# Performance work log

Hardware: AMD Instinct MI355X
Metric: run time of the kernel (lower is better)

Reference implementation:

```python
import jax, jax.numpy as jnp
import numpy as np

SEQ_LEN = 12
E, H, BOTTLE = 64, 128, 1024
G, P = 64, 24
B = G * P
EPS = 1e-12  # F.normalize eps


def setup_inputs() -> dict:
    key = jax.random.key(0)
    ks = jax.random.split(key, 24)
    r = lambda k, s: (jax.random.normal(k, s, dtype=jnp.float32) * 0.1)
    starts = np.arange(G, dtype=np.int64) * P
    seq_start_end = jnp.asarray(np.stack([starts, starts + P], axis=1))
    return {
        'last_pos': jax.random.normal(ks[0], (B, 2), dtype=jnp.float32),
        'last_pos_rel': jax.random.normal(ks[1], (B, 2), dtype=jnp.float32),
        'h0': jax.random.normal(ks[2], (1, B, H), dtype=jnp.float32),
        'c0': jax.random.normal(ks[3], (1, B, H), dtype=jnp.float32),
        'seq_start_end': seq_start_end,
        # decoder spatial embedding Linear(2, E)
        'W_emb': r(ks[4], (E, 2)), 'b_emb': r(ks[5], (E,)),
        # LSTM(E -> H), gates ordered i,f,g,o as in torch
        'W_ih': r(ks[6], (4 * H, E)), 'W_hh': r(ks[7], (4 * H, H)),
        'b_ih': r(ks[8], (4 * H,)), 'b_hh': r(ks[9], (4 * H,)),
        # hidden2pos Linear(H, 2)
        'W_pos': r(ks[10], (2, H)), 'b_pos': r(ks[11], (2,)),
        # pool_net spatial embedding Linear(2, E)
        'Wp_emb': r(ks[12], (E, 2)), 'bp_emb': r(ks[13], (E,)),
        # pool_net mlp_pre_pool: (E+H)->512->1024, ReLU
        'Wp1': r(ks[14], (512, E + H)), 'bp1': r(ks[15], (512,)),
        'Wp2': r(ks[16], (BOTTLE, 512)), 'bp2': r(ks[17], (BOTTLE,)),
        # decoder mlp: (H+BOTTLE)->1024->H, ReLU
        'Wm1': r(ks[18], (1024, H + BOTTLE)), 'bm1': r(ks[19], (1024,)),
        'Wm2': r(ks[20], (H, 1024)), 'bm2': r(ks[21], (H,)),
    }


def reference(last_pos, last_pos_rel, h0, c0, seq_start_end,
              W_emb, b_emb, W_ih, W_hh, b_ih, b_hh, W_pos, b_pos,
              Wp_emb, bp_emb, Wp1, bp1, Wp2, bp2, Wm1, bm1, Wm2, bm2):
    batch = last_pos.shape[0]
    n_grp = seq_start_end.shape[0]
    n_ped = batch // n_grp  # equal contiguous groups -> static reshape
    h_dim = h0.shape[-1]

    def pool_net(h, pos):
        # h: [B,H], pos: [B,2]; groups are contiguous slices of size n_ped
        pos_g = pos.reshape(n_grp, n_ped, 2)
        hid_g = h.reshape(n_grp, n_ped, h_dim)
        # rel[g,i,j] = pos[g,j] - pos[g,i]  (torch repeat semantics)
        rel = pos_g[:, None, :, :] - pos_g[:, :, None, :]  # [G,P,P,2]
        nrm = jnp.linalg.norm(rel, axis=-1, keepdims=True)
        rel = rel / jnp.maximum(nrm, EPS)
        emb = rel @ Wp_emb.T + bp_emb                       # [G,P,P,E]
        hid_b = jnp.broadcast_to(hid_g[:, None, :, :], (n_grp, n_ped, n_ped, h_dim))
        x = jnp.concatenate([emb, hid_b], axis=-1)          # [G,P,P,E+H]
        x = jax.nn.relu(x @ Wp1.T + bp1)
        x = jax.nn.relu(x @ Wp2.T + bp2)                    # [G,P,P,1024]
        return jnp.max(x, axis=2).reshape(batch, -1)        # max over j

    def lstm_step(x, h, c):
        gates = x @ W_ih.T + b_ih + h @ W_hh.T + b_hh
        i, f, g, o = jnp.split(gates, 4, axis=-1)
        c = jax.nn.sigmoid(f) * c + jax.nn.sigmoid(i) * jnp.tanh(g)
        h = jax.nn.sigmoid(o) * jnp.tanh(c)
        return h, c

    def step(carry, _):
        h, c, lp, dec_in = carry
        h, c = lstm_step(dec_in, h, c)
        rel_pos = h @ W_pos.T + b_pos          # [B,2]
        curr_pos = rel_pos + lp
        pool_h = pool_net(h, curr_pos)         # [B,1024]
        dh = jnp.concatenate([h, pool_h], axis=1)
        dh = jax.nn.relu(dh @ Wm1.T + bm1)
        h = jax.nn.relu(dh @ Wm2.T + bm2)      # refreshed hidden state
        dec_in = rel_pos @ W_emb.T + b_emb
        return (h, c, curr_pos, dec_in), rel_pos

    dec_in0 = last_pos_rel @ W_emb.T + b_emb
    (h, c, lp, di), rels = jax.lax.scan(
        step, (h0[0], c0[0], last_pos, dec_in0), None, length=SEQ_LEN)
    return rels, h[None]  # ([seq_len,B,2], [1,B,H])
```

## Files before the change

kernel.cpp:

```cpp
#include <hip/hip_runtime.h>
#include <hip/hip_bf16.h>

typedef __attribute__((ext_vector_type(4))) float f32x4;
typedef __attribute__((ext_vector_type(8))) _Float16 f16x8;

static __device__ __forceinline__ unsigned short h2u(_Float16 h) {
  union { _Float16 h; unsigned short u; } v; v.h = h; return v.u;
}

#define MFMA16(a, b, c) __builtin_amdgcn_mfma_f32_16x16x32_f16(a, b, c, 0, 0, 0)


__global__ void build_wg(const float* __restrict__ W_ih, const float* __restrict__ W_hh,
                         _Float16* __restrict__ Wg) {
  int i = blockIdx.x * 256 + threadIdx.x;
  if (i < 512 * 192) {
    int rp = i / 192, k = i % 192;
    int u = rp >> 2, gate = rp & 3;
    int sr = gate * 128 + u;
    float v = (k < 64) ? W_ih[sr * 64 + k] : W_hh[sr * 128 + (k - 64)];
    _Float16 h = (_Float16)v;
    Wg[i] = h;
    Wg[512 * 192 + i] = (_Float16)(v - (float)h);
  }
}

__global__ void build_wp1b(const float* __restrict__ Wp1, _Float16* __restrict__ W) {
  int i = blockIdx.x * 256 + threadIdx.x;
  if (i < 512 * 128) {
    int r = i >> 7, k = i & 127;
    float v = Wp1[r * 192 + 64 + k];
    _Float16 h = (_Float16)v;
    W[i] = h;
    W[512 * 128 + i] = (_Float16)(v - (float)h);
  }
}

__global__ void refrag_f32(const float* __restrict__ W, _Float16* __restrict__ F,
                           int N, int Kc) {
  int idx = blockIdx.x * 256 + threadIdx.x;
  int total = (N >> 4) * Kc * 64;
  if (idx >= total) return;
  int l = idx & 63;
  int c = (idx >> 6) % Kc;
  int T = (idx >> 6) / Kc;
  int n = T * 16 + (l & 15);
  int k = c * 32 + (l >> 4) * 8;
  int K = Kc * 32;
  const float* src = W + (size_t)n * K + k;
  _Float16* dst = F + ((size_t)((T * Kc + c) * 2) * 64 + l) * 8;
  for (int e = 0; e < 8; e++) {
    float v = src[e];
    _Float16 h = (_Float16)v;
    dst[e] = h;
    dst[512 + e] = (_Float16)(v - (float)h);
  }
}

__global__ void refrag_planes(const _Float16* __restrict__ Ws, size_t plane,
                              _Float16* __restrict__ F, int N, int Kc) {
  int idx = blockIdx.x * 256 + threadIdx.x;
  int total = (N >> 4) * Kc * 64;
  if (idx >= total) return;
  int l = idx & 63;
  int c = (idx >> 6) % Kc;
  int T = (idx >> 6) / Kc;
  int n = T * 16 + (l & 15);
  int k = c * 32 + (l >> 4) * 8;
  int K = Kc * 32;
  const _Float16* src = Ws + (size_t)n * K + k;
  _Float16* dst = F + ((size_t)((T * Kc + c) * 2) * 64 + l) * 8;
  for (int e = 0; e < 8; e++) {
    dst[e] = src[e];
    dst[512 + e] = src[plane + e];
  }
}

__global__ void build_misc(const float* __restrict__ Wp1, const float* __restrict__ Wp_emb,
                           const float* __restrict__ bp_emb, const float* __restrict__ bp1,
                           const float* __restrict__ b_ih, const float* __restrict__ b_hh,
                           float* __restrict__ Uc, float* __restrict__ c1,
                           float* __restrict__ bias_gi) {
  int r = blockIdx.x * 256 + threadIdx.x;
  if (r < 512) {
    float u0 = 0.f, u1 = 0.f, cc = 0.f;
    for (int e = 0; e < 64; e++) {
      float w = Wp1[r * 192 + e];
      u0 += w * Wp_emb[e * 2 + 0];
      u1 += w * Wp_emb[e * 2 + 1];
      cc += w * bp_emb[e];
    }
    Uc[r * 2 + 0] = u0;
    Uc[r * 2 + 1] = u1;
    c1[r] = bp1[r] + cc;
    int u = r >> 2, gate = r & 3;
    bias_gi[r] = b_ih[gate * 128 + u] + b_hh[gate * 128 + u];
  }
}

__global__ void init_state(const float* __restrict__ lp, const float* __restrict__ lpr,
                           const float* __restrict__ h0, const float* __restrict__ c0,
                           const float* __restrict__ W_emb, const float* __restrict__ b_emb,
                           _Float16* __restrict__ A_lstm, size_t PL_AL,
                           float* __restrict__ c_state, float* __restrict__ curr_pos) {
  int row = blockIdx.x;
  int t = threadIdx.x;
  float v;
  if (t < 64) {
    v = lpr[row * 2] * W_emb[t * 2] + lpr[row * 2 + 1] * W_emb[t * 2 + 1] + b_emb[t];
  } else {
    int u = t - 64;
    v = h0[(size_t)row * 128 + u];
    c_state[(size_t)row * 128 + u] = c0[(size_t)row * 128 + u];
  }
  _Float16 h = (_Float16)v;
  A_lstm[(size_t)row * 192 + t] = h;
  A_lstm[PL_AL + (size_t)row * 192 + t] = (_Float16)(v - (float)h);
  if (t < 2) curr_pos[row * 2 + t] = lp[row * 2 + t];
}


template <int K, int RELU>
__global__ __launch_bounds__(256) void gemm_f16f(
    const _Float16* __restrict__ A, size_t aPl, int lda,
    const _Float16* __restrict__ Bf,
    const float* __restrict__ bias,
    float* __restrict__ outF, int ldoF,
    _Float16* __restrict__ outS, size_t oPl, int ldoS) {
  constexpr int Kc = K / 32;
  __shared__ _Float16 Ah[64][40], Al[64][40];
  const int tid = threadIdx.x;
  const int lane = tid & 63;
  const int wid = tid >> 6;
  const int wm = wid & 1, wn = wid >> 1;
  const int m0 = blockIdx.x * 64, n0 = blockIdx.y * 64;

  f32x4 acc[2][2];
#pragma unroll
  for (int a = 0; a < 2; a++)
#pragma unroll
    for (int b = 0; b < 2; b++) acc[a][b] = (f32x4){0.f, 0.f, 0.f, 0.f};

  const int srow = tid >> 2, sc = (tid & 3) * 8;
  const int ar = wm * 32 + (lane & 15);
  const int kk = (lane >> 4) * 8;
  const int T0 = (n0 >> 4) + wn * 2;

  for (int c = 0; c < Kc; c++) {
    const int k0 = c * 32;
    const _Float16* ap = A + (size_t)(m0 + srow) * lda + k0 + sc;
    uint4 avh = *(const uint4*)ap;
    uint4 avl = *(const uint4*)(ap + aPl);
    const _Float16* fb0 = Bf + ((size_t)((T0 * Kc + c) * 2) * 64 + lane) * 8;
    const _Float16* fb1 = Bf + ((size_t)(((T0 + 1) * Kc + c) * 2) * 64 + lane) * 8;
    f16x8 bh0 = *(const f16x8*)fb0, bl0 = *(const f16x8*)(fb0 + 512);
    f16x8 bh1 = *(const f16x8*)fb1, bl1 = *(const f16x8*)(fb1 + 512);
    *(uint4*)&Ah[srow][sc] = avh;
    *(uint4*)&Al[srow][sc] = avl;
    __syncthreads();
    f16x8 ah0 = *(const f16x8*)&Ah[ar][kk];
    f16x8 ah1 = *(const f16x8*)&Ah[ar + 16][kk];
    f16x8 al0 = *(const f16x8*)&Al[ar][kk];
    f16x8 al1 = *(const f16x8*)&Al[ar + 16][kk];
    acc[0][0] = MFMA16(ah0, bh0, acc[0][0]);
    acc[0][0] = MFMA16(ah0, bl0, acc[0][0]);
    acc[0][0] = MFMA16(al0, bh0, acc[0][0]);
    acc[0][1] = MFMA16(ah0, bh1, acc[0][1]);
    acc[0][1] = MFMA16(ah0, bl1, acc[0][1]);
    acc[0][1] = MFMA16(al0, bh1, acc[0][1]);
    acc[1][0] = MFMA16(ah1, bh0, acc[1][0]);
    acc[1][0] = MFMA16(ah1, bl0, acc[1][0]);
    acc[1][0] = MFMA16(al1, bh0, acc[1][0]);
    acc[1][1] = MFMA16(ah1, bh1, acc[1][1]);
    acc[1][1] = MFMA16(ah1, bl1, acc[1][1]);
    acc[1][1] = MFMA16(al1, bh1, acc[1][1]);
    __syncthreads();
  }
#pragma unroll
  for (int mi = 0; mi < 2; mi++)
#pragma unroll
    for (int ni = 0; ni < 2; ni++)
#pragma unroll
      for (int r = 0; r < 4; r++) {
        int row = m0 + wm * 32 + mi * 16 + (lane >> 4) * 4 + r;
        int col = n0 + wn * 32 + ni * 16 + (lane & 15);
        float v = acc[mi][ni][r];
        if (bias) v += bias[col];
        if (RELU) v = fmaxf(v, 0.f);
        if (outF) outF[(size_t)row * ldoF + col] = v;
        if (outS) {
          _Float16 h = (_Float16)v;
          outS[(size_t)row * ldoS + col] = h;
          outS[oPl + (size_t)row * ldoS + col] = (_Float16)(v - (float)h);
        }
      }
}


__global__ __launch_bounds__(256) void gates_lstm(
    const _Float16* __restrict__ A, size_t aPl,
    const _Float16* __restrict__ Bf,
    const float* __restrict__ bias,
    float* __restrict__ c_state,
    _Float16* __restrict__ A_mlp, size_t oPl) {
  constexpr int Kc = 6;
  __shared__ _Float16 Ah[64][40], Al[64][40];
  __shared__ float sacc[64][68];
  const int tid = threadIdx.x;
  const int lane = tid & 63;
  const int wid = tid >> 6;
  const int wm = wid & 1, wn = wid >> 1;
  const int m0 = blockIdx.x * 64, n0 = blockIdx.y * 64;

  f32x4 acc[2][2];
#pragma unroll
  for (int a = 0; a < 2; a++)
#pragma unroll
    for (int b = 0; b < 2; b++) acc[a][b] = (f32x4){0.f, 0.f, 0.f, 0.f};

  const int srow = tid >> 2, sc = (tid & 3) * 8;
  const int ar = wm * 32 + (lane & 15);
  const int kk = (lane >> 4) * 8;
  const int T0 = (n0 >> 4) + wn * 2;

  for (int c = 0; c < Kc; c++) {
    const int k0 = c * 32;
    const _Float16* ap = A + (size_t)(m0 + srow) * 192 + k0 + sc;
    uint4 avh = *(const uint4*)ap;
    uint4 avl = *(const uint4*)(ap + aPl);
    const _Float16* fb0 = Bf + ((size_t)((T0 * Kc + c) * 2) * 64 + lane) * 8;
    const _Float16* fb1 = Bf + ((size_t)(((T0 + 1) * Kc + c) * 2) * 64 + lane) * 8;
    f16x8 bh0 = *(const f16x8*)fb0, bl0 = *(const f16x8*)(fb0 + 512);
    f16x8 bh1 = *(const f16x8*)fb1, bl1 = *(const f16x8*)(fb1 + 512);
    *(uint4*)&Ah[srow][sc] = avh;
    *(uint4*)&Al[srow][sc] = avl;
    __syncthreads();
    f16x8 ah0 = *(const f16x8*)&Ah[ar][kk];
    f16x8 ah1 = *(const f16x8*)&Ah[ar + 16][kk];
    f16x8 al0 = *(const f16x8*)&Al[ar][kk];
    f16x8 al1 = *(const f16x8*)&Al[ar + 16][kk];
    acc[0][0] = MFMA16(ah0, bh0, acc[0][0]);
    acc[0][0] = MFMA16(ah0, bl0, acc[0][0]);
    acc[0][0] = MFMA16(al0, bh0, acc[0][0]);
    acc[0][1] = MFMA16(ah0, bh1, acc[0][1]);
    acc[0][1] = MFMA16(ah0, bl1, acc[0][1]);
    acc[0][1] = MFMA16(al0, bh1, acc[0][1]);
    acc[1][0] = MFMA16(ah1, bh0, acc[1][0]);
    acc[1][0] = MFMA16(ah1, bl0, acc[1][0]);
    acc[1][0] = MFMA16(al1, bh0, acc[1][0]);
    acc[1][1] = MFMA16(ah1, bh1, acc[1][1]);
    acc[1][1] = MFMA16(ah1, bl1, acc[1][1]);
    acc[1][1] = MFMA16(al1, bh1, acc[1][1]);
    __syncthreads();
  }
#pragma unroll
  for (int mi = 0; mi < 2; mi++)
#pragma unroll
    for (int ni = 0; ni < 2; ni++)
#pragma unroll
      for (int r = 0; r < 4; r++) {
        int row_l = wm * 32 + mi * 16 + (lane >> 4) * 4 + r;
        int col_l = wn * 32 + ni * 16 + (lane & 15);
        sacc[row_l][col_l] = acc[mi][ni][r] + bias[n0 + col_l];
      }
  __syncthreads();
  const int n0u = n0 >> 2;
#pragma unroll
  for (int q = 0; q < 4; q++) {
    int cell = q * 256 + tid;
    int r_l = cell >> 4, u_l = cell & 15;
    float gi = sacc[r_l][u_l * 4 + 0];
    float gf = sacc[r_l][u_l * 4 + 1];
    float gg = sacc[r_l][u_l * 4 + 2];
    float go = sacc[r_l][u_l * 4 + 3];
    int row = m0 + r_l, u = n0u + u_l;
    float si = 1.f / (1.f + expf(-gi));
    float sf = 1.f / (1.f + expf(-gf));
    float so = 1.f / (1.f + expf(-go));
    float cst = sf * c_state[(size_t)row * 128 + u] + si * tanhf(gg);
    c_state[(size_t)row * 128 + u] = cst;
    float h = so * tanhf(cst);
    _Float16 hh = (_Float16)h;
    A_mlp[(size_t)row * 1152 + u] = hh;
    A_mlp[oPl + (size_t)row * 1152 + u] = (_Float16)(h - (float)hh);
  }
}


__global__ __launch_bounds__(256) void hpart_pose(
    const _Float16* __restrict__ A, size_t aPl,
    const _Float16* __restrict__ Bf,
    const float* __restrict__ c1,
    float* __restrict__ hpart,
    const float* __restrict__ W_pos, const float* __restrict__ b_pos,
    const float* __restrict__ W_emb, const float* __restrict__ b_emb,
    float* __restrict__ rels_out, float* __restrict__ curr_pos,
    _Float16* __restrict__ A_lstm, size_t alPl) {
  constexpr int Kc = 4;
  __shared__ _Float16 Ah[64][40], Al[64][40];
  __shared__ float srel[64][2];
  const int tid = threadIdx.x;
  const int lane = tid & 63;
  const int wid = tid >> 6;
  const int wm = wid & 1, wn = wid >> 1;
  const int m0 = blockIdx.x * 64, n0 = blockIdx.y * 64;
  const int by0 = (blockIdx.y == 0);

  f32x4 acc[2][2];
#pragma unroll
  for (int a = 0; a < 2; a++)
#pragma unroll
    for (int b = 0; b < 2; b++) acc[a][b] = (f32x4){0.f, 0.f, 0.f, 0.f};

  const int srow = tid >> 2, sc = (tid & 3) * 8;
  const int ar = wm * 32 + (lane & 15);
  const int kk = (lane >> 4) * 8;
  const int T0 = (n0 >> 4) + wn * 2;
  float pp0 = 0.f, pp1 = 0.f;

  for (int c = 0; c < Kc; c++) {
    const int k0 = c * 32;
    const _Float16* ap = A + (size_t)(m0 + srow) * 1152 + k0 + sc;
    uint4 avh = *(const uint4*)ap;
    uint4 avl = *(const uint4*)(ap + aPl);
    if (by0) {
      union { uint4 u; _Float16 f[8]; } uh, ul;
      uh.u = avh; ul.u = avl;
#pragma unroll
      for (int e = 0; e < 8; e++) {
        float hv = (float)uh.f[e] + (float)ul.f[e];
        int k = k0 + sc + e;
        pp0 += hv * W_pos[k];
        pp1 += hv * W_pos[128 + k];
      }
    }
    const _Float16* fb0 = Bf + ((size_t)((T0 * Kc + c) * 2) * 64 + lane) * 8;
    const _Float16* fb1 = Bf + ((size_t)(((T0 + 1) * Kc + c) * 2) * 64 + lane) * 8;
    f16x8 bh0 = *(const f16x8*)fb0, bl0 = *(const f16x8*)(fb0 + 512);
    f16x8 bh1 = *(const f16x8*)fb1, bl1 = *(const f16x8*)(fb1 + 512);
    *(uint4*)&Ah[srow][sc] = avh;
    *(uint4*)&Al[srow][sc] = avl;
    __syncthreads();
    f16x8 ah0 = *(const f16x8*)&Ah[ar][kk];
    f16x8 ah1 = *(const f16x8*)&Ah[ar + 16][kk];
    f16x8 al0 = *(const f16x8*)&Al[ar][kk];
    f16x8 al1 = *(const f16x8*)&Al[ar + 16][kk];
    acc[0][0] = MFMA16(ah0, bh0, acc[0][0]);
    acc[0][0] = MFMA16(ah0, bl0, acc[0][0]);
    acc[0][0] = MFMA16(al0, bh0, acc[0][0]);
    acc[0][1] = MFMA16(ah0, bh1, acc[0][1]);
    acc[0][1] = MFMA16(ah0, bl1, acc[0][1]);
    acc[0][1] = MFMA16(al0, bh1, acc[0][1]);
    acc[1][0] = MFMA16(ah1, bh0, acc[1][0]);
    acc[1][0] = MFMA16(ah1, bl0, acc[1][0]);
    acc[1][0] = MFMA16(al1, bh0, acc[1][0]);
    acc[1][1] = MFMA16(ah1, bh1, acc[1][1]);
    acc[1][1] = MFMA16(ah1, bl1, acc[1][1]);
    acc[1][1] = MFMA16(al1, bh1, acc[1][1]);
    __syncthreads();
  }
#pragma unroll
  for (int mi = 0; mi < 2; mi++)
#pragma unroll
    for (int ni = 0; ni < 2; ni++)
#pragma unroll
      for (int r = 0; r < 4; r++) {
        int row = m0 + wm * 32 + mi * 16 + (lane >> 4) * 4 + r;
        int col = n0 + wn * 32 + ni * 16 + (lane & 15);
        hpart[(size_t)row * 512 + col] = acc[mi][ni][r] + c1[col];
      }
  if (by0) {
    pp0 += __shfl_xor(pp0, 1);
    pp0 += __shfl_xor(pp0, 2);
    pp1 += __shfl_xor(pp1, 1);
    pp1 += __shfl_xor(pp1, 2);
    if ((tid & 3) == 0) {
      int row = m0 + srow;
      float r0 = pp0 + b_pos[0], r1 = pp1 + b_pos[1];
      rels_out[(size_t)row * 2 + 0] = r0;
      rels_out[(size_t)row * 2 + 1] = r1;
      curr_pos[(size_t)row * 2 + 0] += r0;
      curr_pos[(size_t)row * 2 + 1] += r1;
      srel[srow][0] = r0;
      srel[srow][1] = r1;
    }
    __syncthreads();
#pragma unroll
    for (int q = 0; q < 16; q++) {
      int idx = q * 256 + tid;
      int r_l = idx >> 6, cc = idx & 63;
      int row = m0 + r_l;
      float v = srel[r_l][0] * W_emb[cc * 2] + srel[r_l][1] * W_emb[cc * 2 + 1] + b_emb[cc];
      _Float16 hh = (_Float16)v;
      A_lstm[(size_t)row * 192 + cc] = hh;
      A_lstm[alPl + (size_t)row * 192 + cc] = (_Float16)(v - (float)hh);
    }
  }
}


__global__ __launch_bounds__(512) void pool_gemm(
    const float* __restrict__ hpart,
    const float* __restrict__ curr_pos,
    const float* __restrict__ Uc,
    const _Float16* __restrict__ W2f,
    const float* __restrict__ bp2,
    _Float16* __restrict__ A_mlp, size_t oPl) {
  __shared__ _Float16 Ah[96][40];
  __shared__ float Us0[96], Us1[96];
  __shared__ int pool_tile[4][256];
  int b = blockIdx.x;
  int nt = b & 3;
  int it = (b >> 2) % 6;
  int g = b / 24;
  int tid = threadIdx.x;
  int lane = tid & 63, wid = tid >> 6;
  int wm = wid & 1, wn = wid >> 1;

  int* pt = &pool_tile[0][0];
  pt[tid] = 0;
  pt[tid + 512] = 0;

  if (tid < 96) {
    int r = tid;
    int i = it * 4 + r / 24;
    int j = r % 24;
    float pix = curr_pos[(g * 24 + i) * 2 + 0];
    float piy = curr_pos[(g * 24 + i) * 2 + 1];
    float dx = curr_pos[(g * 24 + j) * 2 + 0] - pix;
    float dy = curr_pos[(g * 24 + j) * 2 + 1] - piy;
    float nrm = sqrtf(dx * dx + dy * dy);
    float inv = 1.f / fmaxf(nrm, 1e-12f);
    Us0[r] = dx * inv;
    Us1[r] = dy * inv;
  }

  f32x4 acc[3][4];
#pragma unroll
  for (int a = 0; a < 3; a++)
#pragma unroll
    for (int c = 0; c < 4; c++) acc[a][c] = (f32x4){0.f, 0.f, 0.f, 0.f};

  const int kc = (2 * tid) & 31;
  const int rb = tid >> 4;
  const int j0 = rb % 24, j1 = (rb + 32) % 24, j2 = (rb + 64) % 24;
  const float* hp0 = hpart + ((size_t)(g * 24 + j0)) * 512 + kc;
  const float* hp1 = hpart + ((size_t)(g * 24 + j1)) * 512 + kc;
  const float* hp2 = hpart + ((size_t)(g * 24 + j2)) * 512 + kc;

  for (int c16 = 0; c16 < 16; c16++) {
    const int k0 = c16 * 32;
    f16x8 bh[4], bl[4];
#pragma unroll
    for (int ni = 0; ni < 4; ni++) {
      int T = nt * 16 + wn * 4 + ni;
      const _Float16* fb = W2f + ((size_t)((T * 16 + c16) * 2) * 64 + lane) * 8;
      bh[ni] = *(const f16x8*)fb;
      bl[ni] = *(const f16x8*)(fb + 512);
    }
    float2 q0 = *(const float2*)(hp0 + k0);
    float2 q1 = *(const float2*)(hp1 + k0);
    float2 q2 = *(const float2*)(hp2 + k0);
    float4 uc = *(const float4*)(Uc + (size_t)(k0 + kc) * 2);
    __syncthreads();
    {
      float u0 = Us0[rb], u1 = Us1[rb];
      float v0 = fmaxf(q0.x + u0 * uc.x + u1 * uc.y, 0.f);
      float v1 = fmaxf(q0.y + u0 * uc.z + u1 * uc.w, 0.f);
      *(unsigned int*)&Ah[rb][kc] =
          (unsigned int)h2u((_Float16)v0) | ((unsigned int)h2u((_Float16)v1) << 16);
      u0 = Us0[rb + 32]; u1 = Us1[rb + 32];
      v0 = fmaxf(q1.x + u0 * uc.x + u1 * uc.y, 0.f);
      v1 = fmaxf(q1.y + u0 * uc.z + u1 * uc.w, 0.f);
      *(unsigned int*)&Ah[rb + 32][kc] =
          (unsigned int)h2u((_Float16)v0) | ((unsigned int)h2u((_Float16)v1) << 16);
      u0 = Us0[rb + 64]; u1 = Us1[rb + 64];
      v0 = fmaxf(q2.x + u0 * uc.x + u1 * uc.y, 0.f);
      v1 = fmaxf(q2.y + u0 * uc.z + u1 * uc.w, 0.f);
      *(unsigned int*)&Ah[rb + 64][kc] =
          (unsigned int)h2u((_Float16)v0) | ((unsigned int)h2u((_Float16)v1) << 16);
    }
    __syncthreads();
    const int kk = (lane >> 4) * 8;
    f16x8 ah[3];
#pragma unroll
    for (int mi = 0; mi < 3; mi++) {
      int ar = wm * 48 + mi * 16 + (lane & 15);
      ah[mi] = *(const f16x8*)&Ah[ar][kk];
    }
#pragma unroll
    for (int mi = 0; mi < 3; mi++)
#pragma unroll
      for (int ni = 0; ni < 4; ni++) {
        acc[mi][ni] = MFMA16(ah[mi], bh[ni], acc[mi][ni]);
        acc[mi][ni] = MFMA16(ah[mi], bl[ni], acc[mi][ni]);
      }
  }
  __syncthreads();
#pragma unroll
  for (int mi = 0; mi < 3; mi++)
#pragma unroll
    for (int ni = 0; ni < 4; ni++)
#pragma unroll
      for (int r = 0; r < 4; r++) {
        int rl = wm * 48 + mi * 16 + (lane >> 4) * 4 + r;
        int il = rl / 24;
        int nl = wn * 64 + ni * 16 + (lane & 15);
        float z = fmaxf(acc[mi][ni][r] + bp2[nt * 256 + nl], 0.f);
        atomicMax(&pool_tile[il][nl], __float_as_int(z));
      }
  __syncthreads();
  for (int idx = tid; idx < 1024; idx += 512) {
    int il = idx >> 8, nl = idx & 255;
    int row = g * 24 + it * 4 + il;
    float z = __int_as_float(pool_tile[il][nl]);
    _Float16 h = (_Float16)z;
    A_mlp[(size_t)row * 1152 + 128 + nt * 256 + nl] = h;
    A_mlp[oPl + (size_t)row * 1152 + 128 + nt * 256 + nl] = (_Float16)(z - (float)h);
  }
}


extern "C" void kernel_launch(void* const* d_in, const int* in_sizes, int n_in,
                              void* d_out, int out_size, void* d_ws, size_t ws_size,
                              hipStream_t stream) {
  (void)in_sizes; (void)n_in; (void)out_size; (void)ws_size;
  const float* last_pos     = (const float*)d_in[0];
  const float* last_pos_rel = (const float*)d_in[1];
  const float* h0    = (const float*)d_in[2];
  const float* c0    = (const float*)d_in[3];
  const float* W_emb = (const float*)d_in[5];
  const float* b_emb = (const float*)d_in[6];
  const float* W_ih  = (const float*)d_in[7];
  const float* W_hh  = (const float*)d_in[8];
  const float* b_ih  = (const float*)d_in[9];
  const float* b_hh  = (const float*)d_in[10];
  const float* W_pos = (const float*)d_in[11];
  const float* b_pos = (const float*)d_in[12];
  const float* Wp_emb = (const float*)d_in[13];
  const float* bp_emb = (const float*)d_in[14];
  const float* Wp1 = (const float*)d_in[15];
  const float* bp1 = (const float*)d_in[16];
  const float* Wp2 = (const float*)d_in[17];
  const float* bp2 = (const float*)d_in[18];
  const float* Wm1 = (const float*)d_in[19];
  const float* bm1 = (const float*)d_in[20];
  const float* Wm2 = (const float*)d_in[21];
  const float* bm2 = (const float*)d_in[22];

  const size_t PL_AL = (size_t)1536 * 192;
  const size_t PL_AM = (size_t)1536 * 1152;
  const size_t PL_DH = (size_t)1536 * 1024;

  char* ws = (char*)d_ws;
  size_t off = 0;
  auto alloc = [&](size_t bytes) -> void* {
    void* p = ws + off;
    off = (off + bytes + 255) & ~(size_t)255;
    return p;
  };
  _Float16* Wgi_s  = (_Float16*)alloc((size_t)512 * 192 * 2 * 2);
  _Float16* Wp1b_s = (_Float16*)alloc((size_t)512 * 128 * 2 * 2);
  _Float16* Wgi_f  = (_Float16*)alloc((size_t)32 * 6 * 1024 * 2);
  _Float16* Wp1b_f = (_Float16*)alloc((size_t)32 * 4 * 1024 * 2);
  _Float16* W2f    = (_Float16*)alloc((size_t)64 * 16 * 1024 * 2);
  _Float16* Wm1_f  = (_Float16*)alloc((size_t)64 * 36 * 1024 * 2);
  _Float16* Wm2_f  = (_Float16*)alloc((size_t)8 * 32 * 1024 * 2);
  float* Uc      = (float*)alloc(512 * 2 * 4);
  float* c1      = (float*)alloc(512 * 4);
  float* bias_gi = (float*)alloc(512 * 4);
  _Float16* A_lstm = (_Float16*)alloc(PL_AL * 2 * 2);
  float* c_state = (float*)alloc((size_t)1536 * 128 * 4);
  _Float16* A_mlp = (_Float16*)alloc(PL_AM * 2 * 2);
  float* curr_pos = (float*)alloc(1536 * 2 * 4);
  float* hpart = (float*)alloc((size_t)1536 * 512 * 4);
  _Float16* dh = (_Float16*)alloc(PL_DH * 2 * 2);

  float* rels = (float*)d_out;
  float* h_out = ((float*)d_out) + 12 * 1536 * 2;

  build_wg<<<(98304 + 255) / 256, 256, 0, stream>>>(W_ih, W_hh, Wgi_s);
  build_wp1b<<<(65536 + 255) / 256, 256, 0, stream>>>(Wp1, Wp1b_s);
  refrag_planes<<<(12288 + 255) / 256, 256, 0, stream>>>(Wgi_s, 98304, Wgi_f, 512, 6);
  refrag_planes<<<(8192 + 255) / 256, 256, 0, stream>>>(Wp1b_s, 65536, Wp1b_f, 512, 4);
  refrag_f32<<<(65536 + 255) / 256, 256, 0, stream>>>(Wp2, W2f, 1024, 16);
  refrag_f32<<<(147456 + 255) / 256, 256, 0, stream>>>(Wm1, Wm1_f, 1024, 36);
  refrag_f32<<<(16384 + 255) / 256, 256, 0, stream>>>(Wm2, Wm2_f, 128, 32);
  build_misc<<<2, 256, 0, stream>>>(Wp1, Wp_emb, bp_emb, bp1, b_ih, b_hh, Uc, c1, bias_gi);
  init_state<<<1536, 192, 0, stream>>>(last_pos, last_pos_rel, h0, c0, W_emb, b_emb,
                                       A_lstm, PL_AL, c_state, curr_pos);

  for (int t = 0; t < 12; t++) {
    gates_lstm<<<dim3(24, 8), 256, 0, stream>>>(A_lstm, PL_AL, Wgi_f, bias_gi,
                                                c_state, A_mlp, PL_AM);
    hpart_pose<<<dim3(24, 8), 256, 0, stream>>>(A_mlp, PL_AM, Wp1b_f, c1, hpart,
                                                W_pos, b_pos, W_emb, b_emb,
                                                rels + (size_t)t * 1536 * 2, curr_pos,
                                                A_lstm, PL_AL);
    pool_gemm<<<1536, 512, 0, stream>>>(hpart, curr_pos, Uc, W2f, bp2, A_mlp, PL_AM);
    gemm_f16f<1152, 1><<<dim3(24, 16), 256, 0, stream>>>(
        A_mlp, PL_AM, 1152, Wm1_f, bm1, (float*)nullptr, 0, dh, PL_DH, 1024);
    float* houtF = (t == 11) ? h_out : (float*)nullptr;
    gemm_f16f<1024, 1><<<dim3(24, 2), 256, 0, stream>>>(
        dh, PL_DH, 1024, Wm2_f, bm2, houtF, 128, A_lstm + 64, PL_AL, 192);
  }
}
```

Before: 1.726 ms.

## Double-buffer pool_gemm A tile and stage Uc in shared memory

The pool_gemm K loop now uses two shared A buffers. Each iteration prefetches the next chunk of hpart, runs the MFMAs on the current buffer, then builds the next A tile, so one barrier per iteration replaces two. The Uc projection table is loaded once into shared memory instead of being read from global memory every iteration. In exchange the kernel uses more LDS and holds more live registers for the prefetch, which may reduce occupancy.

```diff
diff --git a/kernel.cpp b/kernel.cpp
--- a/kernel.cpp
+++ b/kernel.cpp
@@ -406,7 +406,8 @@
     const _Float16* __restrict__ W2f,
     const float* __restrict__ bp2,
     _Float16* __restrict__ A_mlp, size_t oPl) {
-  __shared__ _Float16 Ah[96][40];
+  __shared__ _Float16 Ah[2][96][40];
+  __shared__ float4 UcS[256];
   __shared__ float Us0[96], Us1[96];
   __shared__ int pool_tile[4][256];
   int b = blockIdx.x;
@@ -420,6 +421,8 @@
   int* pt = &pool_tile[0][0];
   pt[tid] = 0;
   pt[tid + 512] = 0;
+
+  if (tid < 256) UcS[tid] = ((const float4*)Uc)[tid];
 
   if (tid < 96) {
     int r = tid;
@@ -447,46 +450,53 @@
   const float* hp0 = hpart + ((size_t)(g * 24 + j0)) * 512 + kc;
   const float* hp1 = hpart + ((size_t)(g * 24 + j1)) * 512 + kc;
   const float* hp2 = hpart + ((size_t)(g * 24 + j2)) * 512 + kc;
-
-  for (int c16 = 0; c16 < 16; c16++) {
-    const int k0 = c16 * 32;
+  const int kk = (lane >> 4) * 8;
+
+  float2 q0 = *(const float2*)(hp0);
+  float2 q1 = *(const float2*)(hp1);
+  float2 q2 = *(const float2*)(hp2);
+  __syncthreads();
+  {
+    float4 uc = UcS[kc >> 1];
+    float u0 = Us0[rb], u1 = Us1[rb];
+    float v0 = fmaxf(q0.x + u0 * uc.x + u1 * uc.y, 0.f);
+    float v1 = fmaxf(q0.y + u0 * uc.z + u1 * uc.w, 0.f);
+    *(unsigned int*)&Ah[0][rb][kc] =
+        (unsigned int)h2u((_Float16)v0) | ((unsigned int)h2u((_Float16)v1) << 16);
+    u0 = Us0[rb + 32]; u1 = Us1[rb + 32];
+    v0 = fmaxf(q1.x + u0 * uc.x + u1 * uc.y, 0.f);
+    v1 = fmaxf(q1.y + u0 * uc.z + u1 * uc.w, 0.f);
+    *(unsigned int*)&Ah[0][rb + 32][kc] =
+        (unsigned int)h2u((_Float16)v0) | ((unsigned int)h2u((_Float16)v1) << 16);
+    u0 = Us0[rb + 64]; u1 = Us1[rb + 64];
+    v0 = fmaxf(q2.x + u0 * uc.x + u1 * uc.y, 0.f);
+    v1 = fmaxf(q2.y + u0 * uc.z + u1 * uc.w, 0.f);
+    *(unsigned int*)&Ah[0][rb + 64][kc] =
+        (unsigned int)h2u((_Float16)v0) | ((unsigned int)h2u((_Float16)v1) << 16);
+  }
+  __syncthreads();
+
+  auto iter = [&](int c, int cur, int nxt) {
+    const int k0 = c * 32;
     f16x8 bh[4], bl[4];
 #pragma unroll
     for (int ni = 0; ni < 4; ni++) {
       int T = nt * 16 + wn * 4 + ni;
-      const _Float16* fb = W2f + ((size_t)((T * 16 + c16) * 2) * 64 + lane) * 8;
+      const _Float16* fb = W2f + ((size_t)((T * 16 + c) * 2) * 64 + lane) * 8;
       bh[ni] = *(const f16x8*)fb;
       bl[ni] = *(const f16x8*)(fb + 512);
     }
-    float2 q0 = *(const float2*)(hp0 + k0);
-    float2 q1 = *(const float2*)(hp1 + k0);
-    float2 q2 = *(const float2*)(hp2 + k0);
-    float4 uc = *(const float4*)(Uc + (size_t)(k0 + kc) * 2);
-    __syncthreads();
-    {
-      float u0 = Us0[rb], u1 = Us1[rb];
-      float v0 = fmaxf(q0.x + u0 * uc.x + u1 * uc.y, 0.f);
-      float v1 = fmaxf(q0.y + u0 * uc.z + u1 * uc.w, 0.f);
-      *(unsigned int*)&Ah[rb][kc] =
-          (unsigned int)h2u((_Float16)v0) | ((unsigned int)h2u((_Float16)v1) << 16);
-      u0 = Us0[rb + 32]; u1 = Us1[rb + 32];
-      v0 = fmaxf(q1.x + u0 * uc.x + u1 * uc.y, 0.f);
-      v1 = fmaxf(q1.y + u0 * uc.z + u1 * uc.w, 0.f);
-      *(unsigned int*)&Ah[rb + 32][kc] =
-          (unsigned int)h2u((_Float16)v0) | ((unsigned int)h2u((_Float16)v1) << 16);
-      u0 = Us0[rb + 64]; u1 = Us1[rb + 64];
-      v0 = fmaxf(q2.x + u0 * uc.x + u1 * uc.y, 0.f);
-      v1 = fmaxf(q2.y + u0 * uc.z + u1 * uc.w, 0.f);
-      *(unsigned int*)&Ah[rb + 64][kc] =
-          (unsigned int)h2u((_Float16)v0) | ((unsigned int)h2u((_Float16)v1) << 16);
-    }
-    __syncthreads();
-    const int kk = (lane >> 4) * 8;
+    float2 p0, p1, p2;
+    if (c < 15) {
+      p0 = *(const float2*)(hp0 + k0 + 32);
+      p1 = *(const float2*)(hp1 + k0 + 32);
+      p2 = *(const float2*)(hp2 + k0 + 32);
+    }
     f16x8 ah[3];
 #pragma unroll
     for (int mi = 0; mi < 3; mi++) {
       int ar = wm * 48 + mi * 16 + (lane & 15);
-      ah[mi] = *(const f16x8*)&Ah[ar][kk];
+      ah[mi] = *(const f16x8*)&Ah[cur][ar][kk];
     }
 #pragma unroll
     for (int mi = 0; mi < 3; mi++)
@@ -495,8 +505,32 @@
         acc[mi][ni] = MFMA16(ah[mi], bh[ni], acc[mi][ni]);
         acc[mi][ni] = MFMA16(ah[mi], bl[ni], acc[mi][ni]);
       }
-  }
-  __syncthreads();
+    if (c < 15) {
+      float4 uc = UcS[(k0 + 32 + kc) >> 1];
+      float u0 = Us0[rb], u1 = Us1[rb];
+      float v0 = fmaxf(p0.x + u0 * uc.x + u1 * uc.y, 0.f);
+      float v1 = fmaxf(p0.y + u0 * uc.z + u1 * uc.w, 0.f);
+      *(unsigned int*)&Ah[nxt][rb][kc] =
+          (unsigned int)h2u((_Float16)v0) | ((unsigned int)h2u((_Float16)v1) << 16);
+      u0 = Us0[rb + 32]; u1 = Us1[rb + 32];
+      v0 = fmaxf(p1.x + u0 * uc.x + u1 * uc.y, 0.f);
+      v1 = fmaxf(p1.y + u0 * uc.z + u1 * uc.w, 0.f);
+      *(unsigned int*)&Ah[nxt][rb + 32][kc] =
+          (unsigned int)h2u((_Float16)v0) | ((unsigned int)h2u((_Float16)v1) << 16);
+      u0 = Us0[rb + 64]; u1 = Us1[rb + 64];
+      v0 = fmaxf(p2.x + u0 * uc.x + u1 * uc.y, 0.f);
+      v1 = fmaxf(p2.y + u0 * uc.z + u1 * uc.w, 0.f);
+      *(unsigned int*)&Ah[nxt][rb + 64][kc] =
+          (unsigned int)h2u((_Float16)v0) | ((unsigned int)h2u((_Float16)v1) << 16);
+    }
+    __syncthreads();
+  };
+
+  for (int cc = 0; cc < 16; cc += 2) {
+    iter(cc, 0, 1);
+    iter(cc + 1, 1, 0);
+  }
+
 #pragma unroll
   for (int mi = 0; mi < 3; mi++)
 #pragma unroll
```

Result: slower. 1.905 ms (+10.4%).
